# Kernel optimization log

Measured on AMD Instinct MI355X. Metric: run time of the kernel, lower is better.

## Reference

```python
import jax, jax.numpy as jnp
import numpy as np

N, E, F, H, O = 50000, 1_600_000, 512, 256, 128


def setup_inputs() -> dict:
    key = jax.random.key(0)
    k1, k2, k3, k4, k5 = jax.random.split(key, 5)
    x = jax.random.normal(k1, (N, F), dtype=jnp.float32)
    edge_index = jax.random.randint(k2, (2, E), 0, N, dtype=jnp.int32)
    edge_weight = jax.random.uniform(k3, (E,), dtype=jnp.float32)
    W1 = jax.random.normal(k4, (F, H), dtype=jnp.float32) * (1.0 / np.sqrt(F))
    b1 = jnp.zeros((H,), dtype=jnp.float32)
    W2 = jax.random.normal(k5, (H, O), dtype=jnp.float32) * (1.0 / np.sqrt(H))
    b2 = jnp.zeros((O,), dtype=jnp.float32)
    return {"x": x, "edge_index": edge_index, "edge_weight": edge_weight,
            "W1": W1, "b1": b1, "W2": W2, "b2": b2}


def reference(x, edge_index, edge_weight, W1, b1, W2, b2):
    n = x.shape[0]
    src, dst = edge_index[0], edge_index[1]
    # GCNConv: add self-loops with weight 1
    loop = jnp.arange(n, dtype=src.dtype)
    src = jnp.concatenate([src, loop])
    dst = jnp.concatenate([dst, loop])
    w = jnp.concatenate([edge_weight, jnp.ones((n,), dtype=x.dtype)])
    # symmetric normalization D^{-1/2} (A+I) D^{-1/2}
    deg = jax.ops.segment_sum(w, dst, num_segments=n)
    dinv = jnp.where(deg > 0, jax.lax.rsqrt(deg), 0.0)
    norm = dinv[src] * w * dinv[dst]  # [E+N]

    def conv(h, W, b):
        h = h @ W                                   # linear first (PyG GCNConv)
        msg = h[src] * norm[:, None]                # gather + scale per edge
        return jax.ops.segment_sum(msg, dst, num_segments=n) + b

    h = jax.nn.relu(conv(x, W1, b1))
    return conv(h, W2, b2)
```

## Files before the change

kernel.cpp:

```cpp
#include <hip/hip_runtime.h>
#include <hip/hip_bf16.h>

#define CAP 80
#define NPB 98
#define BCAP 4096
#define CHUNK_E 2048

typedef __attribute__((ext_vector_type(8))) short bf16x8;
typedef __attribute__((ext_vector_type(4))) float f32x4;
typedef __attribute__((ext_vector_type(2))) float f32x2;

__device__ inline ushort f2bf(float f){
  union{float f; unsigned u;} c{f};
  unsigned r = (c.u + 0x7fff + ((c.u>>16)&1)) >> 16;
  return (ushort)r;
}
__device__ inline float blo(unsigned u){ return __uint_as_float(u<<16); }
__device__ inline float bhi(unsigned u){ return __uint_as_float(u & 0xffff0000u); }


__device__ inline unsigned char fp8_enc(float v){
#if __has_builtin(__builtin_amdgcn_cvt_pk_fp8_f32)
  int p = __builtin_amdgcn_cvt_pk_fp8_f32(v, v, 0, false);
  return (unsigned char)(p & 0xff);
#else
  unsigned s = v < 0.f ? 0x80u : 0u;
  float a = fabsf(v);
  if (a >= 448.f) return (unsigned char)(s | 0x7Eu);
  if (a < 7.8125e-3f){
    int m = (int)rintf(a * 512.f); if (m > 15) m = 15;
    if (m >= 8) return (unsigned char)(s | (1u<<3) | (unsigned)(m-8));
    return (unsigned char)(s | (unsigned)m);
  }
  int e; float fr = frexpf(a, &e);
  int m = (int)rintf(fr * 16.f);
  if (m == 16){ m = 8; e++; }
  int ee = e - 1 + 7;
  if (ee > 15) return (unsigned char)(s | 0x7Eu);
  return (unsigned char)(s | (unsigned)(ee<<3) | (unsigned)(m-8));
#endif
}

__device__ inline void fp8x4_dec(unsigned w, float d[4]){
#if __has_builtin(__builtin_amdgcn_cvt_pk_f32_fp8)
  f32x2 lo = __builtin_amdgcn_cvt_pk_f32_fp8((int)w, false);
  f32x2 hi = __builtin_amdgcn_cvt_pk_f32_fp8((int)w, true);
  d[0] = lo[0]; d[1] = lo[1]; d[2] = hi[0]; d[3] = hi[1];
#else
  #pragma unroll
  for (int i = 0; i < 4; ++i){
    unsigned v = (w >> (8*i)) & 0xffu;
    unsigned s = v & 0x80u, e = (v>>3)&15u, m = v&7u;
    float f = e ? ldexpf((float)(8+m), (int)e - 10) : ldexpf((float)m, -9);
    d[i] = s ? -f : f;
  }
#endif
}


__global__ void k_init0(int* a, int n){
  int i = blockIdx.x*blockDim.x + threadIdx.x;
  if (i < n) a[i] = 0;
}


__global__ __launch_bounds__(256) void k_bin(const int* __restrict__ src,
                                             const int* __restrict__ dst,
                                             const float* __restrict__ w,
                                             int* __restrict__ bktcur,
                                             uint2* __restrict__ bkt, int E, int nb){
  __shared__ int hist[512];
  __shared__ int base[512];
  const int t  = threadIdx.x;
  const int c0 = blockIdx.x * CHUNK_E;
  const int cend = min(c0 + CHUNK_E, E);
  for (int i = t; i < nb; i += 256) hist[i] = 0;
  __syncthreads();
  for (int e = c0 + t; e < cend; e += 256)
    atomicAdd(&hist[dst[e]/NPB], 1);
  __syncthreads();
  for (int i = t; i < nb; i += 256){
    int h = hist[i];
    base[i] = (h > 0) ? atomicAdd(&bktcur[i], h) : 0;
    hist[i] = 0;
  }
  __syncthreads();
  for (int e = c0 + t; e < cend; e += 256){
    int d = dst[e];
    int b = d / NPB;
    int pos = base[b] + atomicAdd(&hist[b], 1);
    if (pos < BCAP){
      unsigned lo = ((unsigned)src[e] << 16) | (unsigned)f2bf(w[e]);
      bkt[(size_t)b*BCAP + pos] = make_uint2(lo, (unsigned)d);
    }
  }
}


__global__ __launch_bounds__(256) void k_build(const uint2* __restrict__ bkt,
                                               const int* __restrict__ bktcur,
                                               unsigned* __restrict__ padcsr,
                                               int* __restrict__ cnt,
                                               float* __restrict__ dinv, int N){
  __shared__ unsigned rows[NPB][CAP];
  __shared__ int   lcnt[NPB];
  __shared__ float lws[NPB];
  const int b = blockIdx.x;
  const int t = threadIdx.x;
  const int node0 = b * NPB;
  for (int i = t; i < NPB; i += 256){ lcnt[i] = 0; lws[i] = 0.f; }
  __syncthreads();
  const int cb = min(bktcur[b], BCAP);
  for (int e = t; e < cb; e += 256){
    uint2 rec = bkt[(size_t)b*BCAP + e];
    int ld = (int)rec.y - node0;
    int pos = atomicAdd(&lcnt[ld], 1);
    if (pos < CAP) rows[ld][pos] = rec.x;
    atomicAdd(&lws[ld], blo(rec.x));
  }
  __syncthreads();
  const int maxn = min(NPB, N - node0);
  unsigned* gslice = padcsr + (size_t)node0*CAP;
  const int tot = maxn * CAP;
  const unsigned* lbase = &rows[0][0];
  for (int i = t*4; i < tot; i += 1024)
    *(uint4*)(gslice + i) = *(const uint4*)(lbase + i);
  for (int i = t; i < maxn; i += 256){
    cnt[node0 + i]  = lcnt[i];
    dinv[node0 + i] = rsqrtf(1.f + lws[i]);
  }
}


__global__ __launch_bounds__(256, 2) void gemm1_f8(const float* __restrict__ X,
                                                   const float* __restrict__ Wm,
                                                   unsigned char* __restrict__ out, int M){
  __shared__ short As[128][56];
  __shared__ short Bs[256][56];
  const int t    = threadIdx.x;
  const int lane = t & 63;
  const int wave = t >> 6;
  const int wr   = wave >> 1;
  const int wc   = wave & 1;
  const int i0   = blockIdx.x * 128;

  f32x4 acc[4][8];
  #pragma unroll
  for (int m = 0; m < 4; ++m)
    #pragma unroll
    for (int nn = 0; nn < 8; ++nn)
      acc[m][nn] = (f32x4){0.f,0.f,0.f,0.f};

  const int arow = t >> 1;
  const int akh  = (t & 1) * 16;

  for (int kt = 0; kt < 512; kt += 32){
    {
      int gi = i0 + arow;
      ushort hv[16];
      if (gi < M){
        const float4* ap4 = (const float4*)(X + (size_t)gi*512 + kt + akh);
        #pragma unroll
        for (int q = 0; q < 4; ++q){
          float4 v = ap4[q];
          hv[q*4+0] = f2bf(v.x); hv[q*4+1] = f2bf(v.y);
          hv[q*4+2] = f2bf(v.z); hv[q*4+3] = f2bf(v.w);
        }
      } else {
        #pragma unroll
        for (int q = 0; q < 16; ++q) hv[q] = 0;
      }
      *(uint4*)&As[arow][akh]     = *(uint4*)&hv[0];
      *(uint4*)&As[arow][akh + 8] = *(uint4*)&hv[8];
    }
    {
      #pragma unroll
      for (int s2 = 0; s2 < 4; ++s2){
        int s  = t + s2*256;
        int bn = s & 255;
        int k8 = s >> 8;
        ushort hv[8];
        #pragma unroll
        for (int i = 0; i < 8; ++i){
          float v = Wm[(size_t)(kt + k8*8 + i)*256 + bn];
          hv[i] = f2bf(v);
        }
        *(uint4*)&Bs[bn][k8*8] = *(uint4*)&hv[0];
      }
    }
    __syncthreads();
    bf16x8 a_f[4], b_f[8];
    #pragma unroll
    for (int m = 0; m < 4; ++m)
      a_f[m] = *(bf16x8*)&As[wr*64 + m*16 + (lane & 15)][(lane >> 4) * 8];
    #pragma unroll
    for (int nn = 0; nn < 8; ++nn)
      b_f[nn] = *(bf16x8*)&Bs[wc*128 + nn*16 + (lane & 15)][(lane >> 4) * 8];
    #pragma unroll
    for (int m = 0; m < 4; ++m)
      #pragma unroll
      for (int nn = 0; nn < 8; ++nn)
        acc[m][nn] = __builtin_amdgcn_mfma_f32_16x16x32_bf16(a_f[m], b_f[nn], acc[m][nn], 0, 0, 0);
    __syncthreads();
  }
  #pragma unroll
  for (int m = 0; m < 4; ++m){
    int r_base = i0 + wr*64 + m*16 + ((lane >> 4) << 2);
    #pragma unroll
    for (int nn = 0; nn < 8; ++nn){
      int c = wc*128 + nn*16 + (lane & 15);
      #pragma unroll
      for (int r = 0; r < 4; ++r){
        int gr = r_base + r;
        if (gr < M) out[(size_t)gr*256 + c] = fp8_enc(acc[m][nn][r]);
      }
    }
  }
}


template<typename TIN, int K, int DOUT>
__global__ __launch_bounds__(256) void mfma_gemm(const TIN* __restrict__ X,
                                                 const float* __restrict__ Wm,
                                                 ushort* __restrict__ out, int M){
  __shared__ short As[128][56];
  __shared__ short Bs[128][56];
  const int t    = threadIdx.x;
  const int lane = t & 63;
  const int wave = t >> 6;
  const int wr   = wave >> 1;
  const int wc   = wave & 1;
  const int i0   = blockIdx.x * 128;
  const int n0   = blockIdx.y * 128;

  f32x4 acc[4][4];
  #pragma unroll
  for (int m = 0; m < 4; ++m)
    #pragma unroll
    for (int nn = 0; nn < 4; ++nn)
      acc[m][nn] = (f32x4){0.f,0.f,0.f,0.f};

  const int arow = t >> 1;
  const int akh  = (t & 1) * 16;

  for (int kt = 0; kt < K; kt += 32){
    {
      int gi = i0 + arow;
      ushort hv[16];
      if (gi < M){
        const uint4* ap4 = (const uint4*)(X + (size_t)gi*K + kt + akh);
        uint4 u0 = ap4[0], u1 = ap4[1];
        *(uint4*)&hv[0] = u0; *(uint4*)&hv[8] = u1;
      } else {
        #pragma unroll
        for (int q = 0; q < 16; ++q) hv[q] = 0;
      }
      *(uint4*)&As[arow][akh]     = *(uint4*)&hv[0];
      *(uint4*)&As[arow][akh + 8] = *(uint4*)&hv[8];
    }
    {
      #pragma unroll
      for (int s2 = 0; s2 < 2; ++s2){
        int s  = t + s2*256;
        int bn = s & 127;
        int k8 = s >> 7;
        ushort hv[8];
        #pragma unroll
        for (int i = 0; i < 8; ++i){
          float v = Wm[(size_t)(kt + k8*8 + i)*DOUT + n0 + bn];
          hv[i] = f2bf(v);
        }
        *(uint4*)&Bs[bn][k8*8] = *(uint4*)&hv[0];
      }
    }
    __syncthreads();
    bf16x8 a_f[4], b_f[4];
    #pragma unroll
    for (int m = 0; m < 4; ++m)
      a_f[m] = *(bf16x8*)&As[wr*64 + m*16 + (lane & 15)][(lane >> 4) * 8];
    #pragma unroll
    for (int nn = 0; nn < 4; ++nn)
      b_f[nn] = *(bf16x8*)&Bs[wc*64 + nn*16 + (lane & 15)][(lane >> 4) * 8];
    #pragma unroll
    for (int m = 0; m < 4; ++m)
      #pragma unroll
      for (int nn = 0; nn < 4; ++nn)
        acc[m][nn] = __builtin_amdgcn_mfma_f32_16x16x32_bf16(a_f[m], b_f[nn], acc[m][nn], 0, 0, 0);
    __syncthreads();
  }
  #pragma unroll
  for (int m = 0; m < 4; ++m){
    int r_base = i0 + wr*64 + m*16 + ((lane >> 4) << 2);
    #pragma unroll
    for (int nn = 0; nn < 4; ++nn){
      int c = n0 + wc*64 + nn*16 + (lane & 15);
      #pragma unroll
      for (int r = 0; r < 4; ++r){
        int gr = r_base + r;
        if (gr < M) out[(size_t)gr*DOUT + c] = f2bf(acc[m][nn][r]);
      }
    }
  }
}


__global__ __launch_bounds__(256) void agg_fp8(const unsigned char* __restrict__ tin,
                                               const int* __restrict__ cnt,
                                               const unsigned* __restrict__ padcsr,
                                               const float* __restrict__ dinv,
                                               const float* __restrict__ bias,
                                               ushort* __restrict__ outp, int n){
  constexpr int U = 4;
  int node = blockIdx.x*4 + (threadIdx.x >> 6);
  if (node >= n) return;
  int lane = threadIdx.x & 63;
  int sl   = lane & 15;
  int part = lane >> 4;
  const size_t boff = (size_t)sl * 16;
  const unsigned* row = padcsr + (size_t)node*CAP;

  float acc[16];
  #pragma unroll
  for (int i = 0; i < 16; ++i) acc[i] = 0.f;
  int len = min(cnt[node], CAP);
  int e = 0;
  for (; e + 4*U <= len; e += 4*U){
    int srcs[U]; float ws[U];
    #pragma unroll
    for (int u = 0; u < U; ++u){
      unsigned rec = row[e + u*4 + part];
      srcs[u] = (int)(rec >> 16); ws[u] = blo(rec);
    }
    float dv[U];
    #pragma unroll
    for (int u = 0; u < U; ++u) dv[u] = dinv[srcs[u]];
    uint4 g[U];
    #pragma unroll
    for (int u = 0; u < U; ++u) g[u] = *(const uint4*)(tin + (size_t)srcs[u]*256 + boff);
    #pragma unroll
    for (int u = 0; u < U; ++u){
      float w = ws[u] * dv[u];
      float d[4];
      fp8x4_dec(g[u].x, d);
      acc[0]  += d[0]*w; acc[1]  += d[1]*w; acc[2]  += d[2]*w; acc[3]  += d[3]*w;
      fp8x4_dec(g[u].y, d);
      acc[4]  += d[0]*w; acc[5]  += d[1]*w; acc[6]  += d[2]*w; acc[7]  += d[3]*w;
      fp8x4_dec(g[u].z, d);
      acc[8]  += d[0]*w; acc[9]  += d[1]*w; acc[10] += d[2]*w; acc[11] += d[3]*w;
      fp8x4_dec(g[u].w, d);
      acc[12] += d[0]*w; acc[13] += d[1]*w; acc[14] += d[2]*w; acc[15] += d[3]*w;
    }
  }
  for (; e < len; e += 4){
    int idx = e + part;
    int s = node; float w = 0.f;
    if (idx < len){ unsigned rec = row[idx]; s = (int)(rec >> 16); w = blo(rec) * dinv[s]; }
    uint4 g = *(const uint4*)(tin + (size_t)s*256 + boff);
    float d[4];
    fp8x4_dec(g.x, d);
    acc[0]  += d[0]*w; acc[1]  += d[1]*w; acc[2]  += d[2]*w; acc[3]  += d[3]*w;
    fp8x4_dec(g.y, d);
    acc[4]  += d[0]*w; acc[5]  += d[1]*w; acc[6]  += d[2]*w; acc[7]  += d[3]*w;
    fp8x4_dec(g.z, d);
    acc[8]  += d[0]*w; acc[9]  += d[1]*w; acc[10] += d[2]*w; acc[11] += d[3]*w;
    fp8x4_dec(g.w, d);
    acc[12] += d[0]*w; acc[13] += d[1]*w; acc[14] += d[2]*w; acc[15] += d[3]*w;
  }
  #pragma unroll
  for (int i = 0; i < 16; ++i){
    acc[i] += __shfl_xor(acc[i], 16);
    acc[i] += __shfl_xor(acc[i], 32);
  }
  if (part == 0){
    float di = dinv[node];
    uint4 gs = *(const uint4*)(tin + (size_t)node*256 + boff);
    float d[4];
    fp8x4_dec(gs.x, d);
    acc[0]  += d[0]*di; acc[1]  += d[1]*di; acc[2]  += d[2]*di; acc[3]  += d[3]*di;
    fp8x4_dec(gs.y, d);
    acc[4]  += d[0]*di; acc[5]  += d[1]*di; acc[6]  += d[2]*di; acc[7]  += d[3]*di;
    fp8x4_dec(gs.z, d);
    acc[8]  += d[0]*di; acc[9]  += d[1]*di; acc[10] += d[2]*di; acc[11] += d[3]*di;
    fp8x4_dec(gs.w, d);
    acc[12] += d[0]*di; acc[13] += d[1]*di; acc[14] += d[2]*di; acc[15] += d[3]*di;
    ushort hv[16];
    #pragma unroll
    for (int q = 0; q < 4; ++q){
      float4 bq = *(const float4*)(bias + sl*16 + q*4);
      acc[q*4+0] = acc[q*4+0]*di + bq.x;
      acc[q*4+1] = acc[q*4+1]*di + bq.y;
      acc[q*4+2] = acc[q*4+2]*di + bq.z;
      acc[q*4+3] = acc[q*4+3]*di + bq.w;
    }
    #pragma unroll
    for (int i = 0; i < 16; ++i) hv[i] = f2bf(fmaxf(acc[i], 0.f));
    ushort* op = outp + (size_t)node*256 + sl*16;
    *(uint4*)op       = *(uint4*)&hv[0];
    *(uint4*)(op + 8) = *(uint4*)&hv[8];
  }
}


template<int D, int MODE>
__global__ __launch_bounds__(256) void agg_pad(const ushort* __restrict__ tin,
                                               const int* __restrict__ cnt,
                                               const unsigned* __restrict__ padcsr,
                                               const float* __restrict__ dinv,
                                               const float* __restrict__ bias,
                                               void* __restrict__ outp, int n){
  constexpr int LPR = D/8;
  constexpr int EPW = 64/LPR;
  constexpr int U   = 4;
  int node = blockIdx.x*4 + (threadIdx.x >> 6);
  if (node >= n) return;
  int lane = threadIdx.x & 63;
  int sl   = lane & (LPR-1);
  int part = lane / LPR;
  const size_t boff = (size_t)sl*8;
  const unsigned* row = padcsr + (size_t)node*CAP;

  float acc[8] = {0,0,0,0,0,0,0,0};
  int len = min(cnt[node], CAP);
  int e = 0;
  for (; e + EPW*U <= len; e += EPW*U){
    int srcs[U]; float ws[U];
    #pragma unroll
    for (int u = 0; u < U; ++u){
      unsigned rec = row[e + u*EPW + part];
      srcs[u] = (int)(rec >> 16); ws[u] = blo(rec);
    }
    float dv[U];
    #pragma unroll
    for (int u = 0; u < U; ++u) dv[u] = dinv[srcs[u]];
    uint4 g[U];
    #pragma unroll
    for (int u = 0; u < U; ++u) g[u] = *(const uint4*)(tin + (size_t)srcs[u]*D + boff);
    #pragma unroll
    for (int u = 0; u < U; ++u){
      float w = ws[u] * dv[u];
      acc[0] += blo(g[u].x)*w; acc[1] += bhi(g[u].x)*w;
      acc[2] += blo(g[u].y)*w; acc[3] += bhi(g[u].y)*w;
      acc[4] += blo(g[u].z)*w; acc[5] += bhi(g[u].z)*w;
      acc[6] += blo(g[u].w)*w; acc[7] += bhi(g[u].w)*w;
    }
  }
  for (; e < len; e += EPW){
    int idx = e + part;
    int s = node; float w = 0.f;
    if (idx < len){
      unsigned rec = row[idx];
      s = (int)(rec >> 16);
      w = blo(rec) * dinv[s];
    }
    uint4 g = *(const uint4*)(tin + (size_t)s*D + boff);
    acc[0] += blo(g.x)*w; acc[1] += bhi(g.x)*w;
    acc[2] += blo(g.y)*w; acc[3] += bhi(g.y)*w;
    acc[4] += blo(g.z)*w; acc[5] += bhi(g.z)*w;
    acc[6] += blo(g.w)*w; acc[7] += bhi(g.w)*w;
  }
  #pragma unroll
  for (int i = 0; i < 8; ++i){
    if constexpr (EPW == 4) acc[i] += __shfl_xor(acc[i], 16);
    acc[i] += __shfl_xor(acc[i], 32);
  }
  if (part == 0){
    float di = dinv[node];
    uint4 gs = *(const uint4*)(tin + (size_t)node*D + boff);
    acc[0] += blo(gs.x)*di; acc[1] += bhi(gs.x)*di;
    acc[2] += blo(gs.y)*di; acc[3] += bhi(gs.y)*di;
    acc[4] += blo(gs.z)*di; acc[5] += bhi(gs.z)*di;
    acc[6] += blo(gs.w)*di; acc[7] += bhi(gs.w)*di;
    float4 b0 = *(const float4*)(bias + sl*8);
    float4 b1 = *(const float4*)(bias + sl*8 + 4);
    acc[0] = acc[0]*di + b0.x; acc[1] = acc[1]*di + b0.y;
    acc[2] = acc[2]*di + b0.z; acc[3] = acc[3]*di + b0.w;
    acc[4] = acc[4]*di + b1.x; acc[5] = acc[5]*di + b1.y;
    acc[6] = acc[6]*di + b1.z; acc[7] = acc[7]*di + b1.w;
    if constexpr (MODE == 0){
      ushort hv[8];
      #pragma unroll
      for (int i = 0; i < 8; ++i) hv[i] = f2bf(fmaxf(acc[i], 0.f));
      *(uint4*)((ushort*)outp + (size_t)node*D + boff) = *(uint4*)&hv[0];
    } else {
      float* op = (float*)outp + (size_t)node*D + boff;
      *(float4*)op     = make_float4(acc[0],acc[1],acc[2],acc[3]);
      *(float4*)(op+4) = make_float4(acc[4],acc[5],acc[6],acc[7]);
    }
  }
}


static inline size_t align_up(size_t x){ return (x + 255) & ~(size_t)255; }

extern "C" void kernel_launch(void* const* d_in, const int* in_sizes, int n_in,
                              void* d_out, int out_size, void* d_ws, size_t ws_size,
                              hipStream_t stream){
  const float* x   = (const float*)d_in[0];
  const int*   ei  = (const int*)  d_in[1];
  const float* ew  = (const float*)d_in[2];
  const float* W1  = (const float*)d_in[3];
  const float* b1  = (const float*)d_in[4];
  const float* W2  = (const float*)d_in[5];
  const float* b2  = (const float*)d_in[6];

  const int H = in_sizes[4];
  const int F = in_sizes[3] / H;
  const int N = in_sizes[0] / F;
  const int E = in_sizes[2];

  const int* src = ei;
  const int* dst = ei + E;

  const int nb = (N + NPB - 1) / NPB;

  char* p = (char*)d_ws;
  int*      cnt     = (int*)p;            p += align_up((size_t)N*4);
  float*    dinv    = (float*)p;          p += align_up((size_t)N*4);
  int*      bktcur  = (int*)p;            p += align_up((size_t)nb*4);
  unsigned* padcsr  = (unsigned*)p;       p += align_up((size_t)N*CAP*4);
  unsigned char* t1 = (unsigned char*)p;  p += align_up((size_t)N*H);
  uint2*    bkt     = (uint2*)p;
  ushort*   h1      = (ushort*)p;         p += align_up((size_t)N*H*2 > (size_t)nb*BCAP*8 ?
                                                        (size_t)N*H*2 : (size_t)nb*BCAP*8);
  ushort*   t2      = (ushort*)t1;

  hipLaunchKernelGGL(k_init0, dim3((nb+255)/256), dim3(256), 0, stream, bktcur, nb);
  hipLaunchKernelGGL(k_bin, dim3((E+CHUNK_E-1)/CHUNK_E), dim3(256), 0, stream,
                     src, dst, ew, bktcur, bkt, E, nb);
  hipLaunchKernelGGL(k_build, dim3(nb), dim3(256), 0, stream,
                     bkt, bktcur, padcsr, cnt, dinv, N);

  hipLaunchKernelGGL(gemm1_f8, dim3((N+127)/128), dim3(256), 0, stream, x, W1, t1, N);
  hipLaunchKernelGGL(agg_fp8, dim3((N+3)/4), dim3(256), 0, stream,
                     t1, cnt, padcsr, dinv, b1, h1, N);

  hipLaunchKernelGGL((mfma_gemm<__hip_bfloat16,256,128>), dim3((N+127)/128, 1), dim3(256), 0, stream,
                     (const __hip_bfloat16*)h1, W2, t2, N);
  hipLaunchKernelGGL((agg_pad<128,1>), dim3((N+3)/4), dim3(256), 0, stream,
                     t2, cnt, padcsr, dinv, b2, d_out, N);
}
```

Measured before the change: 242.2 us.

## Vectorize edge binning loads, add occupancy hint to GEMM, use memset for init

The binning kernel now loads dst, src and weight as int4/float4, eight edges per thread, for full chunks. It keeps them in registers across both the histogram and scatter passes, so the edge arrays are not re-read from global memory. The bf16 GEMM gets a launch-bounds minimum of two blocks per CU, and the small init kernel is replaced with hipMemsetAsync. The vector loads assume 16-byte alignment of the dst slice, which holds only when E is a multiple of four, and the code guards on that. Holding the edges in registers adds register pressure in k_bin.

```diff
diff --git a/kernel.cpp b/kernel.cpp
--- a/kernel.cpp
+++ b/kernel.cpp
@@ -58,12 +58,6 @@
 }
 
 
-__global__ void k_init0(int* a, int n){
-  int i = blockIdx.x*blockDim.x + threadIdx.x;
-  if (i < n) a[i] = 0;
-}
-
-
 __global__ __launch_bounds__(256) void k_bin(const int* __restrict__ src,
                                              const int* __restrict__ dst,
                                              const float* __restrict__ w,
@@ -76,8 +70,25 @@
   const int cend = min(c0 + CHUNK_E, E);
   for (int i = t; i < nb; i += 256) hist[i] = 0;
   __syncthreads();
-  for (int e = c0 + t; e < cend; e += 256)
-    atomicAdd(&hist[dst[e]/NPB], 1);
+  const bool full = ((cend - c0) == CHUNK_E) && ((E & 3) == 0);
+  int4 d4[2], s4[2]; float4 w4[2];
+  if (full){
+    const int e0 = c0 + t*8;
+    #pragma unroll
+    for (int q = 0; q < 2; ++q){
+      d4[q] = *(const int4*)(dst + e0 + q*4);
+      s4[q] = *(const int4*)(src + e0 + q*4);
+      w4[q] = *(const float4*)(w  + e0 + q*4);
+    }
+    #pragma unroll
+    for (int q = 0; q < 2; ++q){
+      atomicAdd(&hist[d4[q].x/NPB],1); atomicAdd(&hist[d4[q].y/NPB],1);
+      atomicAdd(&hist[d4[q].z/NPB],1); atomicAdd(&hist[d4[q].w/NPB],1);
+    }
+  } else {
+    for (int e = c0 + t; e < cend; e += 256)
+      atomicAdd(&hist[dst[e]/NPB], 1);
+  }
   __syncthreads();
   for (int i = t; i < nb; i += 256){
     int h = hist[i];
@@ -85,13 +96,31 @@
     hist[i] = 0;
   }
   __syncthreads();
-  for (int e = c0 + t; e < cend; e += 256){
-    int d = dst[e];
-    int b = d / NPB;
-    int pos = base[b] + atomicAdd(&hist[b], 1);
-    if (pos < BCAP){
-      unsigned lo = ((unsigned)src[e] << 16) | (unsigned)f2bf(w[e]);
-      bkt[(size_t)b*BCAP + pos] = make_uint2(lo, (unsigned)d);
+  if (full){
+    #pragma unroll
+    for (int q = 0; q < 2; ++q){
+      int   dd[4] = {d4[q].x, d4[q].y, d4[q].z, d4[q].w};
+      int   ss[4] = {s4[q].x, s4[q].y, s4[q].z, s4[q].w};
+      float ww[4] = {w4[q].x, w4[q].y, w4[q].z, w4[q].w};
+      #pragma unroll
+      for (int j = 0; j < 4; ++j){
+        int b = dd[j] / NPB;
+        int pos = base[b] + atomicAdd(&hist[b], 1);
+        if (pos < BCAP){
+          unsigned lo = ((unsigned)ss[j] << 16) | (unsigned)f2bf(ww[j]);
+          bkt[(size_t)b*BCAP + pos] = make_uint2(lo, (unsigned)dd[j]);
+        }
+      }
+    }
+  } else {
+    for (int e = c0 + t; e < cend; e += 256){
+      int d = dst[e];
+      int b = d / NPB;
+      int pos = base[b] + atomicAdd(&hist[b], 1);
+      if (pos < BCAP){
+        unsigned lo = ((unsigned)src[e] << 16) | (unsigned)f2bf(w[e]);
+        bkt[(size_t)b*BCAP + pos] = make_uint2(lo, (unsigned)d);
+      }
     }
   }
 }
@@ -220,9 +249,9 @@
 
 
 template<typename TIN, int K, int DOUT>
-__global__ __launch_bounds__(256) void mfma_gemm(const TIN* __restrict__ X,
-                                                 const float* __restrict__ Wm,
-                                                 ushort* __restrict__ out, int M){
+__global__ __launch_bounds__(256, 2) void mfma_gemm(const TIN* __restrict__ X,
+                                                    const float* __restrict__ Wm,
+                                                    ushort* __restrict__ out, int M){
   __shared__ short As[128][56];
   __shared__ short Bs[128][56];
   const int t    = threadIdx.x;
@@ -524,7 +553,7 @@
                                                         (size_t)N*H*2 : (size_t)nb*BCAP*8);
   ushort*   t2      = (ushort*)t1;
 
-  hipLaunchKernelGGL(k_init0, dim3((nb+255)/256), dim3(256), 0, stream, bktcur, nb);
+  hipMemsetAsync(bktcur, 0, (size_t)nb*4, stream);
   hipLaunchKernelGGL(k_bin, dim3((E+CHUNK_E-1)/CHUNK_E), dim3(256), 0, stream,
                      src, dst, ew, bktcur, bkt, E, nb);
   hipLaunchKernelGGL(k_build, dim3(nb), dim3(256), 0, stream,
```

Measured after the change: 241.2 us. Within noise of the previous version (-0.4%).
